# Kernel optimization log

Hardware: AMD Instinct MI355X
Metric: run time of the kernel (lower is better)

The kernel has to match this reference:

```python
import jax, jax.numpy as jnp
import numpy as np

H, W, D_F, N, BINS = 64, 64, 768, 16, 16
SPAN = 1.0
CLIP = 3.0


def _make_bin_idx(h, w, bins):
    # torch _fftfreq_1d == np.fft.fftfreq (k/n with negative wrap)
    fx = np.fft.fftfreq(h).astype(np.float32)
    fy = np.fft.fftfreq(w).astype(np.float32)
    r = np.sqrt(fx[:, None] ** 2 + fy[None, :] ** 2)  # (h, w)
    edges = np.linspace(r.min(), r.max() + 1e-12, bins + 1, dtype=np.float32)
    # torch.bucketize(r, edges[1:-1], right=False) == searchsorted side='left'
    idx = np.searchsorted(edges[1:-1], r, side='left')
    return np.clip(idx, 0, bins - 1).astype(np.int32)


def setup_inputs() -> dict:
    key = jax.random.key(0)
    x = jax.random.normal(key, (N, D_F, H, W), dtype=jnp.float32)
    # parameter init exactly as torch __init__ (bins>1, span>0 branch)
    g_init = np.linspace(-SPAN, SPAN, BINS, dtype=np.float32)
    deltas = np.clip(g_init[1:] - g_init[:-1], 1e-6, None)
    raw_deltas = np.log(np.expm1(deltas)).astype(np.float32)  # inverse softplus
    g1 = np.float32(g_init[0])
    bin_idx_2d = _make_bin_idx(H, W, BINS)
    return {
        "x": x,
        "g1": jnp.asarray(g1),
        "raw_deltas": jnp.asarray(raw_deltas),
        "bin_idx_2d": jnp.asarray(bin_idx_2d),
    }


def _sqrt_lambda(g1, raw_deltas, bin_idx_2d):
    # monotone bin values g_b = g1 + cumsum(softplus(raw_deltas))
    deltas = jax.nn.softplus(raw_deltas)
    g = jnp.concatenate([g1[None], g1[None] + jnp.cumsum(deltas)], axis=0)  # (bins,)
    ell = g[bin_idx_2d]                      # (h, w) log-lambda per frequency
    ell = ell - ell.mean()                   # logdet gauge centering
    ell = jnp.clip(ell, -CLIP, CLIP)
    lam = jnp.exp(ell)
    # logdet gauge: normalize geometric mean to 1 (clip may break centering)
    lam = lam / jnp.maximum(jnp.exp(jnp.log(lam).mean()), 1e-12)
    return jnp.sqrt(lam)


def reference(x, g1, raw_deltas, bin_idx_2d):
    sqrt_lam = _sqrt_lambda(g1, raw_deltas, bin_idx_2d).astype(x.dtype)
    X = jnp.fft.fft2(x, norm="ortho")                    # (n, d_f, h, w) complex
    y = jnp.fft.ifft2(X * sqrt_lam[None, None, :, :], norm="ortho").real
    return y.astype(x.dtype)
```

## Files before the change

### kernel.cpp

```cpp
#include <hip/hip_runtime.h>
#include <math.h>


#define ST 66

__device__ __forceinline__ float2 cadd(float2 a, float2 b){ return make_float2(a.x+b.x, a.y+b.y); }
__device__ __forceinline__ float2 csub(float2 a, float2 b){ return make_float2(a.x-b.x, a.y-b.y); }
__device__ __forceinline__ float2 cmul(float2 a, float2 b){ return make_float2(a.x*b.x - a.y*b.y, a.x*b.y + a.y*b.x); }
__device__ __forceinline__ float2 cmulc(float2 a, float2 b){
  return make_float2(a.x*b.x + a.y*b.y, a.y*b.x - a.x*b.y);
}

template<int SGN>
__device__ __forceinline__ float2 crot(float2 a){
  return (SGN < 0) ? make_float2(a.y, -a.x) : make_float2(-a.y, a.x);
}

template<int SGN>
__device__ __forceinline__ void fft8(float2 a[8]){
  const float s = 0.70710678118654752440f;
  float2 e0=a[0], e1=a[2], e2=a[4], e3=a[6];
  float2 o0=a[1], o1=a[3], o2=a[5], o3=a[7];
  float2 t0=cadd(e0,e2), t1=csub(e0,e2), t2=cadd(e1,e3), t3=crot<SGN>(csub(e1,e3));
  float2 E0=cadd(t0,t2), E2=csub(t0,t2), E1=cadd(t1,t3), E3=csub(t1,t3);
  float2 u0=cadd(o0,o2), u1=csub(o0,o2), u2=cadd(o1,o3), u3=crot<SGN>(csub(o1,o3));
  float2 O0=cadd(u0,u2), O2=csub(u0,u2), O1=cadd(u1,u3), O3=csub(u1,u3);
  const float2 w1 = make_float2( s, (SGN < 0) ? -s : s);
  const float2 w3 = make_float2(-s, (SGN < 0) ? -s : s);
  O1 = cmul(O1, w1);
  O2 = crot<SGN>(O2);
  O3 = cmul(O3, w3);
  a[0]=cadd(E0,O0); a[4]=csub(E0,O0);
  a[1]=cadd(E1,O1); a[5]=csub(E1,O1);
  a[2]=cadd(E2,O2); a[6]=csub(E2,O2);
  a[3]=cadd(E3,O3); a[7]=csub(E3,O3);
}

__device__ __forceinline__ void lds_sync(){
  __builtin_amdgcn_fence(__ATOMIC_ACQ_REL, "wavefront");
  __builtin_amdgcn_wave_barrier();
  __builtin_amdgcn_fence(__ATOMIC_ACQ_REL, "wavefront");
}

__global__ void filter_kernel(const float* __restrict__ g1p,
                              const float* __restrict__ rawd,
                              const int*   __restrict__ bidx,
                              float*       __restrict__ Sperm){
  __shared__ float gsh[16];
  __shared__ float red[256];
  const int tid = threadIdx.x;
  if (tid == 0){
    float g = g1p[0];
    gsh[0] = g;
    for (int b = 0; b < 15; ++b){
      float d = rawd[b];
      float sp = (d > 20.f) ? d : log1pf(expf(d));
      g += sp;
      gsh[b+1] = g;
    }
  }
  __syncthreads();
  float ell[16];
  float sacc = 0.f;
  #pragma unroll
  for (int i = 0; i < 16; ++i){
    int p = tid + 256*i;
    ell[i] = gsh[bidx[p]];
    sacc += ell[i];
  }
  red[tid] = sacc; __syncthreads();
  for (int off = 128; off > 0; off >>= 1){
    if (tid < off) red[tid] += red[tid + off];
    __syncthreads();
  }
  float mean1 = red[0] * (1.f/4096.f);
  __syncthreads();
  sacc = 0.f;
  #pragma unroll
  for (int i = 0; i < 16; ++i){
    float e = ell[i] - mean1;
    e = fminf(fmaxf(e, -3.f), 3.f);
    ell[i] = e;
    sacc += e;
  }
  red[tid] = sacc; __syncthreads();
  for (int off = 128; off > 0; off >>= 1){
    if (tid < off) red[tid] += red[tid + off];
    __syncthreads();
  }
  float mean2 = red[0] * (1.f/4096.f);
  #pragma unroll
  for (int i = 0; i < 16; ++i){
    int p = tid + 256*i;
    int h = p >> 6, w = p & 63;
    float val = expf(0.5f * (ell[i] - mean2)) * (1.0f/4096.0f);
    int ph = ((h & 7) << 3) | (h >> 3);
    int pw = ((w & 7) << 3) | (w >> 3);
    Sperm[ph*64 + pw] = val;
  }
}

__global__ __launch_bounds__(512) void spectral_kernel(
    const float* __restrict__ x, const float* __restrict__ Sp, float* __restrict__ y)
{
  __shared__ float2 tile[64*ST];
  __shared__ float2 twl[64];
  const int tid = threadIdx.x;
  const long long baseA = (long long)blockIdx.x * 8192;
  const float* xA = x + baseA;
  const float* xB = xA + 4096;
  float* yA = y + baseA;
  float* yB = yA + 4096;

  if (tid < 64){
    int n1 = tid >> 3, k2 = tid & 7;
    float ang = -(float)M_PI * (float)(n1 * k2) / 32.0f;
    float sv, cv;
    __sincosf(ang, &sv, &cv);
    twl[tid] = make_float2(cv, sv);
  }

  #pragma unroll
  for (int q = 0; q < 2; ++q){
    int f = tid + q*512;
    int row = f >> 4, g = (f & 15) << 2;
    float4 va = ((const float4*)xA)[f];
    float4 vb = ((const float4*)xB)[f];
    int m = row & 15, rb = row * ST;
    tile[rb + ((g+0) ^ m)] = make_float2(va.x, vb.x);
    tile[rb + ((g+1) ^ m)] = make_float2(va.y, vb.y);
    tile[rb + ((g+2) ^ m)] = make_float2(va.z, vb.z);
    tile[rb + ((g+3) ^ m)] = make_float2(va.w, vb.w);
  }
  __syncthreads();

  {
    const int r = tid >> 3, t = tid & 7;
    const int rb = r * ST, m = r & 15;
    float2 a[8];
    #pragma unroll
    for (int j = 0; j < 8; ++j) a[j] = tile[rb + ((t + 8*j) ^ m)];
    fft8<-1>(a);
    #pragma unroll
    for (int j = 0; j < 8; ++j) a[j] = cmul(a[j], twl[t*8 + j]);
    lds_sync();
    #pragma unroll
    for (int j = 0; j < 8; ++j) tile[rb + ((8*t + j) ^ m)] = a[j];
    lds_sync();
  }
  {
    const int r = tid >> 3, t = tid & 7;
    const int rb = r * ST, m = r & 15;
    float2 a[8];
    #pragma unroll
    for (int j = 0; j < 8; ++j) a[j] = tile[rb + ((8*j + t) ^ m)];
    fft8<-1>(a);
    lds_sync();
    #pragma unroll
    for (int j = 0; j < 8; ++j) tile[rb + ((8*t + j) ^ m)] = a[j];
  }
  __syncthreads();

  {
    const int c = tid >> 3, t = tid & 7;
    float2 a[8];
    #pragma unroll
    for (int j = 0; j < 8; ++j){ int i = t + 8*j; a[j] = tile[i*ST + (c ^ (i & 15))]; }
    fft8<-1>(a);
    #pragma unroll
    for (int j = 0; j < 8; ++j) a[j] = cmul(a[j], twl[t*8 + j]);
    lds_sync();
    #pragma unroll
    for (int j = 0; j < 8; ++j){ int i = 8*t + j; tile[i*ST + (c ^ (i & 15))] = a[j]; }
    lds_sync();
  }
  {
    const int c = tid >> 3, t = tid & 7;
    float2 a[8];
    #pragma unroll
    for (int j = 0; j < 8; ++j){ int i = 8*j + t; a[j] = tile[i*ST + (c ^ (i & 15))]; }
    fft8<-1>(a);
    lds_sync();
    #pragma unroll
    for (int j = 0; j < 8; ++j){ int i = 8*t + j; tile[i*ST + (c ^ (i & 15))] = a[j]; }
    lds_sync();
  }

  {
    const int c = tid >> 3, t = tid & 7;
    float2 a[8];
    #pragma unroll
    for (int j = 0; j < 8; ++j){
      int i = 8*t + j;
      float sc = Sp[i*64 + c];
      float2 v = tile[i*ST + (c ^ (i & 15))];
      a[j] = make_float2(v.x*sc, v.y*sc);
    }
    fft8<+1>(a);
    #pragma unroll
    for (int j = 0; j < 8; ++j) a[j] = cmulc(a[j], twl[j*8 + t]);
    lds_sync();
    #pragma unroll
    for (int j = 0; j < 8; ++j){ int i = t + 8*j; tile[i*ST + (c ^ (i & 15))] = a[j]; }
    lds_sync();
  }
  {
    const int c = tid >> 3, t = tid & 7;
    float2 a[8];
    #pragma unroll
    for (int j = 0; j < 8; ++j){ int i = j + 8*t; a[j] = tile[i*ST + (c ^ (i & 15))]; }
    fft8<+1>(a);
    lds_sync();
    #pragma unroll
    for (int j = 0; j < 8; ++j){ int i = t + 8*j; tile[i*ST + (c ^ (i & 15))] = a[j]; }
  }
  __syncthreads();

  {
    const int r = tid >> 3, t = tid & 7;
    const int rb = r * ST, m = r & 15;
    float2 a[8];
    #pragma unroll
    for (int j = 0; j < 8; ++j) a[j] = tile[rb + ((8*t + j) ^ m)];
    fft8<+1>(a);
    #pragma unroll
    for (int j = 0; j < 8; ++j) a[j] = cmulc(a[j], twl[j*8 + t]);
    lds_sync();
    #pragma unroll
    for (int j = 0; j < 8; ++j) tile[rb + ((t + 8*j) ^ m)] = a[j];
    lds_sync();
  }
  {
    const int r = tid >> 3, t = tid & 7;
    const int rb = r * ST, m = r & 15;
    float2 a[8];
    #pragma unroll
    for (int j = 0; j < 8; ++j) a[j] = tile[rb + ((j + 8*t) ^ m)];
    fft8<+1>(a);
    lds_sync();
    #pragma unroll
    for (int j = 0; j < 8; ++j) tile[rb + ((t + 8*j) ^ m)] = a[j];
  }
  __syncthreads();

  #pragma unroll
  for (int q = 0; q < 2; ++q){
    int f = tid + q*512;
    int row = f >> 4, g = (f & 15) << 2;
    int m = row & 15, rb = row * ST;
    float2 v0 = tile[rb + ((g+0) ^ m)];
    float2 v1 = tile[rb + ((g+1) ^ m)];
    float2 v2 = tile[rb + ((g+2) ^ m)];
    float2 v3 = tile[rb + ((g+3) ^ m)];
    ((float4*)yA)[f] = make_float4(v0.x, v1.x, v2.x, v3.x);
    ((float4*)yB)[f] = make_float4(v0.y, v1.y, v2.y, v3.y);
  }
}

extern "C" void kernel_launch(void* const* d_in, const int* in_sizes, int n_in,
                              void* d_out, int out_size, void* d_ws, size_t ws_size,
                              hipStream_t stream){
  (void)in_sizes; (void)n_in; (void)out_size; (void)ws_size;
  const float* x    = (const float*)d_in[0];
  const float* g1   = (const float*)d_in[1];
  const float* rawd = (const float*)d_in[2];
  const int*   bidx = (const int*)d_in[3];
  float* y     = (float*)d_out;
  float* Sperm = (float*)d_ws;

  filter_kernel<<<dim3(1), dim3(256), 0, stream>>>(g1, rawd, bidx, Sperm);
  spectral_kernel<<<dim3(6144), dim3(512), 0, stream>>>(x, Sperm, y);
}
```

Before: 396.6 us.

## Restructure 2D FFT kernel: direct global loads, fused column pass, register twiddles

Row FFTs now read straight from global memory into registers and write results straight back, which removes the initial and final LDS staging passes. The column forward FFT, filter multiply and column inverse FFT are fused in one phase, and the filter layout changes to match the new digit ordering. Twiddles are kept in registers (computed with sincos per thread) instead of an LDS table, and LDS stores use float4 with a 33-float4 padded stride in place of the XOR swizzle. The per-thread strided scalar global loads and stores may coalesce worse than the old float4 accesses, and launch bounds now request 4 blocks per CU.

Result: faster. 360.7 us (-9.1%).

```diff
diff --git a/kernel.cpp b/kernel.cpp
--- a/kernel.cpp
+++ b/kernel.cpp
@@ -1,8 +1,6 @@
 #include <hip/hip_runtime.h>
 #include <math.h>
 
-
-#define ST 66
 
 __device__ __forceinline__ float2 cadd(float2 a, float2 b){ return make_float2(a.x+b.x, a.y+b.y); }
 __device__ __forceinline__ float2 csub(float2 a, float2 b){ return make_float2(a.x-b.x, a.y-b.y); }
@@ -94,166 +92,118 @@
     int p = tid + 256*i;
     int h = p >> 6, w = p & 63;
     float val = expf(0.5f * (ell[i] - mean2)) * (1.0f/4096.0f);
-    int ph = ((h & 7) << 3) | (h >> 3);
     int pw = ((w & 7) << 3) | (w >> 3);
-    Sperm[ph*64 + pw] = val;
-  }
-}
-
-__global__ __launch_bounds__(512) void spectral_kernel(
+    Sperm[h*64 + pw] = val;
+  }
+}
+
+__global__ __launch_bounds__(512, 4) void spectral_kernel(
     const float* __restrict__ x, const float* __restrict__ Sp, float* __restrict__ y)
 {
-  __shared__ float2 tile[64*ST];
-  __shared__ float2 twl[64];
+  __shared__ float2 tile[64*66];
+  float4* tile4 = reinterpret_cast<float4*>(tile);
   const int tid = threadIdx.x;
+  const int g = tid >> 3;
+  const int t = tid & 7;
   const long long baseA = (long long)blockIdx.x * 8192;
   const float* xA = x + baseA;
   const float* xB = xA + 4096;
   float* yA = y + baseA;
   float* yB = yA + 4096;
 
-  if (tid < 64){
-    int n1 = tid >> 3, k2 = tid & 7;
-    float ang = -(float)M_PI * (float)(n1 * k2) / 32.0f;
+  float2 tw[8];
+  #pragma unroll
+  for (int j = 0; j < 8; ++j){
     float sv, cv;
-    __sincosf(ang, &sv, &cv);
-    twl[tid] = make_float2(cv, sv);
-  }
-
-  #pragma unroll
-  for (int q = 0; q < 2; ++q){
-    int f = tid + q*512;
-    int row = f >> 4, g = (f & 15) << 2;
-    float4 va = ((const float4*)xA)[f];
-    float4 vb = ((const float4*)xB)[f];
-    int m = row & 15, rb = row * ST;
-    tile[rb + ((g+0) ^ m)] = make_float2(va.x, vb.x);
-    tile[rb + ((g+1) ^ m)] = make_float2(va.y, vb.y);
-    tile[rb + ((g+2) ^ m)] = make_float2(va.z, vb.z);
-    tile[rb + ((g+3) ^ m)] = make_float2(va.w, vb.w);
-  }
-  __syncthreads();
+    __sincosf(-(float)M_PI * (float)(t*j) / 32.0f, &sv, &cv);
+    tw[j] = make_float2(cv, sv);
+  }
 
   {
-    const int r = tid >> 3, t = tid & 7;
-    const int rb = r * ST, m = r & 15;
+    const float* rA = xA + (g << 6);
+    const float* rB = xB + (g << 6);
     float2 a[8];
     #pragma unroll
-    for (int j = 0; j < 8; ++j) a[j] = tile[rb + ((t + 8*j) ^ m)];
-    fft8<-1>(a);
-    #pragma unroll
-    for (int j = 0; j < 8; ++j) a[j] = cmul(a[j], twl[t*8 + j]);
-    lds_sync();
-    #pragma unroll
-    for (int j = 0; j < 8; ++j) tile[rb + ((8*t + j) ^ m)] = a[j];
-    lds_sync();
-  }
+    for (int j = 0; j < 8; ++j) a[j] = make_float2(rA[t + 8*j], rB[t + 8*j]);
+    fft8<-1>(a);
+    #pragma unroll
+    for (int j = 1; j < 8; ++j) a[j] = cmul(a[j], tw[j]);
+    #pragma unroll
+    for (int q = 0; q < 4; ++q)
+      tile4[33*g + 4*t + q] = make_float4(a[2*q].x, a[2*q].y, a[2*q+1].x, a[2*q+1].y);
+    lds_sync();
+    #pragma unroll
+    for (int j = 0; j < 8; ++j) a[j] = tile[66*g + 8*j + t];
+    fft8<-1>(a);
+    lds_sync();
+    #pragma unroll
+    for (int q = 0; q < 4; ++q)
+      tile4[33*g + 4*t + q] = make_float4(a[2*q].x, a[2*q].y, a[2*q+1].x, a[2*q+1].y);
+  }
+  __syncthreads();
+
   {
-    const int r = tid >> 3, t = tid & 7;
-    const int rb = r * ST, m = r & 15;
+    const int c = g;
+    const int d = c & 7, Wv = c >> 3;
     float2 a[8];
     #pragma unroll
-    for (int j = 0; j < 8; ++j) a[j] = tile[rb + ((8*j + t) ^ m)];
-    fft8<-1>(a);
-    lds_sync();
-    #pragma unroll
-    for (int j = 0; j < 8; ++j) tile[rb + ((8*t + j) ^ m)] = a[j];
+    for (int j = 0; j < 8; ++j) a[j] = tile[66*(t + 8*j) + c];
+    fft8<-1>(a);
+    #pragma unroll
+    for (int j = 1; j < 8; ++j) a[j] = cmul(a[j], tw[j]);
+    lds_sync();
+    #pragma unroll
+    for (int q = 0; q < 4; ++q)
+      tile4[33*(8*t + d) + 4*Wv + q] = make_float4(a[2*q].x, a[2*q].y, a[2*q+1].x, a[2*q+1].y);
+    lds_sync();
+    #pragma unroll
+    for (int j = 0; j < 8; ++j) a[j] = tile[66*(8*j + d) + 8*Wv + t];
+    fft8<-1>(a);
+    #pragma unroll
+    for (int j = 0; j < 8; ++j){
+      float f = Sp[((t + 8*j) << 6) + c];
+      a[j].x *= f; a[j].y *= f;
+    }
+    fft8<+1>(a);
+    #pragma unroll
+    for (int j = 1; j < 8; ++j) a[j] = cmulc(a[j], tw[j]);
+    lds_sync();
+    #pragma unroll
+    for (int q = 0; q < 4; ++q)
+      tile4[33*(8*t + d) + 4*Wv + q] = make_float4(a[2*q].x, a[2*q].y, a[2*q+1].x, a[2*q+1].y);
+    lds_sync();
+    #pragma unroll
+    for (int j = 0; j < 8; ++j) a[j] = tile[66*(8*j + d) + 8*Wv + t];
+    fft8<+1>(a);
+    lds_sync();
+    #pragma unroll
+    for (int j = 0; j < 8; ++j) tile[66*(t + 8*j) + c] = a[j];
   }
   __syncthreads();
 
   {
-    const int c = tid >> 3, t = tid & 7;
     float2 a[8];
     #pragma unroll
-    for (int j = 0; j < 8; ++j){ int i = t + 8*j; a[j] = tile[i*ST + (c ^ (i & 15))]; }
-    fft8<-1>(a);
-    #pragma unroll
-    for (int j = 0; j < 8; ++j) a[j] = cmul(a[j], twl[t*8 + j]);
-    lds_sync();
-    #pragma unroll
-    for (int j = 0; j < 8; ++j){ int i = 8*t + j; tile[i*ST + (c ^ (i & 15))] = a[j]; }
-    lds_sync();
-  }
-  {
-    const int c = tid >> 3, t = tid & 7;
-    float2 a[8];
-    #pragma unroll
-    for (int j = 0; j < 8; ++j){ int i = 8*j + t; a[j] = tile[i*ST + (c ^ (i & 15))]; }
-    fft8<-1>(a);
-    lds_sync();
-    #pragma unroll
-    for (int j = 0; j < 8; ++j){ int i = 8*t + j; tile[i*ST + (c ^ (i & 15))] = a[j]; }
-    lds_sync();
-  }
-
-  {
-    const int c = tid >> 3, t = tid & 7;
-    float2 a[8];
-    #pragma unroll
-    for (int j = 0; j < 8; ++j){
-      int i = 8*t + j;
-      float sc = Sp[i*64 + c];
-      float2 v = tile[i*ST + (c ^ (i & 15))];
-      a[j] = make_float2(v.x*sc, v.y*sc);
+    for (int q = 0; q < 4; ++q){
+      float4 v = tile4[33*g + 4*t + q];
+      a[2*q]   = make_float2(v.x, v.y);
+      a[2*q+1] = make_float2(v.z, v.w);
     }
     fft8<+1>(a);
     #pragma unroll
-    for (int j = 0; j < 8; ++j) a[j] = cmulc(a[j], twl[j*8 + t]);
-    lds_sync();
-    #pragma unroll
-    for (int j = 0; j < 8; ++j){ int i = t + 8*j; tile[i*ST + (c ^ (i & 15))] = a[j]; }
-    lds_sync();
-  }
-  {
-    const int c = tid >> 3, t = tid & 7;
-    float2 a[8];
-    #pragma unroll
-    for (int j = 0; j < 8; ++j){ int i = j + 8*t; a[j] = tile[i*ST + (c ^ (i & 15))]; }
-    fft8<+1>(a);
-    lds_sync();
-    #pragma unroll
-    for (int j = 0; j < 8; ++j){ int i = t + 8*j; tile[i*ST + (c ^ (i & 15))] = a[j]; }
-  }
-  __syncthreads();
-
-  {
-    const int r = tid >> 3, t = tid & 7;
-    const int rb = r * ST, m = r & 15;
-    float2 a[8];
-    #pragma unroll
-    for (int j = 0; j < 8; ++j) a[j] = tile[rb + ((8*t + j) ^ m)];
-    fft8<+1>(a);
-    #pragma unroll
-    for (int j = 0; j < 8; ++j) a[j] = cmulc(a[j], twl[j*8 + t]);
-    lds_sync();
-    #pragma unroll
-    for (int j = 0; j < 8; ++j) tile[rb + ((t + 8*j) ^ m)] = a[j];
-    lds_sync();
-  }
-  {
-    const int r = tid >> 3, t = tid & 7;
-    const int rb = r * ST, m = r & 15;
-    float2 a[8];
-    #pragma unroll
-    for (int j = 0; j < 8; ++j) a[j] = tile[rb + ((j + 8*t) ^ m)];
-    fft8<+1>(a);
-    lds_sync();
-    #pragma unroll
-    for (int j = 0; j < 8; ++j) tile[rb + ((t + 8*j) ^ m)] = a[j];
-  }
-  __syncthreads();
-
-  #pragma unroll
-  for (int q = 0; q < 2; ++q){
-    int f = tid + q*512;
-    int row = f >> 4, g = (f & 15) << 2;
-    int m = row & 15, rb = row * ST;
-    float2 v0 = tile[rb + ((g+0) ^ m)];
-    float2 v1 = tile[rb + ((g+1) ^ m)];
-    float2 v2 = tile[rb + ((g+2) ^ m)];
-    float2 v3 = tile[rb + ((g+3) ^ m)];
-    ((float4*)yA)[f] = make_float4(v0.x, v1.x, v2.x, v3.x);
-    ((float4*)yB)[f] = make_float4(v0.y, v1.y, v2.y, v3.y);
+    for (int j = 1; j < 8; ++j) a[j] = cmulc(a[j], tw[j]);
+    lds_sync();
+    #pragma unroll
+    for (int q = 0; q < 4; ++q)
+      tile4[33*g + 4*t + q] = make_float4(a[2*q].x, a[2*q].y, a[2*q+1].x, a[2*q+1].y);
+    lds_sync();
+    #pragma unroll
+    for (int j = 0; j < 8; ++j) a[j] = tile[66*g + 8*j + t];
+    fft8<+1>(a);
+    float* wA = yA + (g << 6) + t;
+    float* wB = yB + (g << 6) + t;
+    #pragma unroll
+    for (int j = 0; j < 8; ++j){ wA[8*j] = a[j].x; wB[8*j] = a[j].y; }
   }
 }
 
```
